# Kernel tuning notes

Hardware: AMD Instinct MI355X
Metric: run time of the kernel (lower is better)

## Reference

```python
import jax, jax.numpy as jnp
import numpy as np

VOCAB, X_SIZE, H_SIZE, N_CLASSES = 50000, 300, 150, 5
DEPTH = 18                      # complete binary tree, N = 2^(DEPTH+1)-1 nodes
N_NODES = 2 ** (DEPTH + 1) - 1  # 524287
SCALE = 0.05                    # param init scale for numerical sanity


def setup_inputs() -> dict:
    key = jax.random.key(0)
    ks = jax.random.split(key, 8)
    return {
        "x_id": jax.random.randint(ks[0], (N_NODES,), 0, VOCAB, dtype=jnp.int32),
        "emb": jax.random.normal(ks[1], (VOCAB, X_SIZE), jnp.float32) * SCALE,
        "W_iou": jax.random.normal(ks[2], (X_SIZE, 3 * H_SIZE), jnp.float32) * SCALE,
        "U_iou": jax.random.normal(ks[3], (H_SIZE, 3 * H_SIZE), jnp.float32) * SCALE,
        "b_iou": jnp.zeros((3 * H_SIZE,), jnp.float32),
        "W_f": jax.random.normal(ks[4], (X_SIZE, H_SIZE), jnp.float32) * SCALE,
        "U_f": jax.random.normal(ks[5], (H_SIZE, H_SIZE), jnp.float32) * SCALE,
        "b_f": jnp.zeros((H_SIZE,), jnp.float32),
        "W_out": jax.random.normal(ks[6], (H_SIZE, N_CLASSES), jnp.float32) * SCALE,
        "b_out": jnp.zeros((N_CLASSES,), jnp.float32),
    }


def reference(x_id, emb, W_iou, U_iou, b_iou, W_f, U_f, b_f, W_out, b_out):
    # Child-Sum TreeLSTM propagated leaves->root over a complete binary tree
    # stored in heap layout: children of node i are 2i+1, 2i+2.
    N = x_id.shape[0]
    H = U_iou.shape[0]
    depth = int(np.log2(N + 1)) - 1

    x = emb[x_id]  # input_module: embedding lookup  [N, X]
    h = jnp.zeros((N, H), x.dtype)
    c = jnp.zeros((N, H), x.dtype)

    # level-batched topological propagation (19 static levels)
    for lvl in range(depth, -1, -1):
        s, e = 2 ** lvl - 1, 2 ** (lvl + 1) - 1  # node range of this level
        xl = x[s:e]                              # [n_l, X]
        if lvl == depth:  # leaves: zero child state
            h_sum = jnp.zeros((e - s, H), x.dtype)
            fc_sum = jnp.zeros((e - s, H), x.dtype)
        else:
            # children of consecutive nodes are contiguous: [2s+1, 2e+1)
            hc = h[2 * s + 1:2 * e + 1].reshape(e - s, 2, H)
            cc = c[2 * s + 1:2 * e + 1].reshape(e - s, 2, H)
            h_sum = hc.sum(axis=1)               # reduce: sum child h
            # per-child forget gate
            f = jax.nn.sigmoid((xl @ W_f)[:, None, :] + hc @ U_f + b_f)
            fc_sum = (f * cc).sum(axis=1)
        iou = xl @ W_iou + h_sum @ U_iou + b_iou  # [n_l, 3H]
        i, o, u = jnp.split(iou, 3, axis=-1)
        c_new = jax.nn.sigmoid(i) * jnp.tanh(u) + fc_sum
        h_new = jax.nn.sigmoid(o) * jnp.tanh(c_new)
        h = h.at[s:e].set(h_new)
        c = c.at[s:e].set(c_new)

    return h @ W_out + b_out  # output_module: Linear(H, C)  [N, C]
```

## Files before the change

kernel.cpp:

```cpp
#include <hip/hip_runtime.h>
#include <cstdint>

typedef _Float16 f16_t;
typedef __attribute__((ext_vector_type(8))) _Float16 f16x8;
typedef __attribute__((ext_vector_type(4))) _Float16 f16x4;
typedef __attribute__((ext_vector_type(4))) float f32x4;

#define HP      160
#define NCOL    640
#define KXP     320
#define NNODES  524287
#define LEAF_S  262143
#define NVOCAB  50000
#define AST     168
#define BST     36
#define CST     162

__device__ __forceinline__ float frcp(float x) { return __builtin_amdgcn_rcpf(x); }
__device__ __forceinline__ float sigf(float x) { return frcp(1.0f + __expf(-x)); }
__device__ __forceinline__ float tanhf_(float x) {
  return 1.0f - 2.0f * frcp(1.0f + __expf(2.0f * x));
}
__device__ __forceinline__ f16x8 zero8() {
  f16x8 z;
#pragma unroll
  for (int i = 0; i < 8; ++i) z[i] = (_Float16)0.0f;
  return z;
}
__device__ __forceinline__ f32x4 zero4() {
  f32x4 z;
#pragma unroll
  for (int i = 0; i < 4; ++i) z[i] = 0.0f;
  return z;
}

__device__ __forceinline__ void stage_B(const f16_t* __restrict__ UreT, f16_t* B_sh,
                                        int tid, int j0, int kk) {
#pragma unroll
  for (int i = 0; i < 2; ++i) {
    int ch = tid + 256 * i;
    int cidx = ch >> 2, kc = (ch & 3) * 8;
    int g = cidx >> 5, jj = cidx & 31;
    int col = g * HP + j0 + jj;
    f16x8 v = *(const f16x8*)&UreT[col * HP + kk + kc];
    f16x4 lo = {v[0], v[1], v[2], v[3]};
    f16x4 hi = {v[4], v[5], v[6], v[7]};
    *(f16x4*)&B_sh[cidx * BST + kc] = lo;
    *(f16x4*)&B_sh[cidx * BST + kc + 4] = hi;
  }
}
__device__ __forceinline__ f16x8 read_B(const f16_t* B_sh, int tile16, int q) {
  f16x4 lo = *(const f16x4*)&B_sh[tile16 * BST + q * 8];
  f16x4 hi = *(const f16x4*)&B_sh[tile16 * BST + q * 8 + 4];
  f16x8 v = {lo[0], lo[1], lo[2], lo[3], hi[0], hi[1], hi[2], hi[3]};
  return v;
}

__global__ void prep_params(const float* __restrict__ W_iou, const float* __restrict__ U_iou,
                            const float* __restrict__ b_iou, const float* __restrict__ W_f,
                            const float* __restrict__ U_f, const float* __restrict__ b_f,
                            f16_t* __restrict__ WreT, f16_t* __restrict__ UreT,
                            float* __restrict__ bre) {
  int idx = blockIdx.x * 256 + threadIdx.x;
  if (idx < NCOL * KXP) {
    int col = idx / KXP, k = idx % KXP;
    int j = col >> 2, g = col & 3;
    float v = 0.0f;
    if (k < 300 && j < 150) v = (g < 3) ? W_iou[k * 450 + g * 150 + j] : W_f[k * 150 + j];
    WreT[idx] = (f16_t)v;
  } else if (idx < NCOL * KXP + NCOL * HP) {
    int i2 = idx - NCOL * KXP;
    int col = i2 / HP, k = i2 % HP;
    int g = col / 160, j = col % 160;
    float v = 0.0f;
    if (k < 150 && j < 150) v = (g < 3) ? U_iou[k * 450 + g * 150 + j] : U_f[k * 150 + j];
    UreT[i2] = (f16_t)v;
  } else if (idx < NCOL * KXP + NCOL * HP + NCOL) {
    int col = idx - (NCOL * KXP + NCOL * HP);
    int j = col >> 2, g = col & 3;
    bre[col] = (j < 150) ? ((g < 3) ? b_iou[g * 150 + j] : b_f[j]) : 0.0f;
  }
}

__global__ __launch_bounds__(256) void gemm_p(const float* __restrict__ emb,
                                              const f16_t* __restrict__ WreT,
                                              const float* __restrict__ bre,
                                              f16_t* __restrict__ P) {
  __shared__ __align__(16) f16_t A_sh[64 * 328];
  __shared__ __align__(16) f16_t B_sh[128 * 40];
  const int tid = threadIdx.x;
  const int wid = tid >> 6, lane = tid & 63, l15 = lane & 15, q = lane >> 4;
  const int row0 = blockIdx.x * 64;

#pragma unroll
  for (int i = 0; i < 10; ++i) {
    int ch = tid + 256 * i;
    int r = ch / 40, kc = (ch % 40) * 8;
    int grow = row0 + r;
    f16x8 hv;
    if (grow < NVOCAB && kc + 8 <= 300) {
      float4 a = *(const float4*)&emb[grow * 300 + kc];
      float4 b = *(const float4*)&emb[grow * 300 + kc + 4];
      hv[0] = (_Float16)a.x; hv[1] = (_Float16)a.y; hv[2] = (_Float16)a.z; hv[3] = (_Float16)a.w;
      hv[4] = (_Float16)b.x; hv[5] = (_Float16)b.y; hv[6] = (_Float16)b.z; hv[7] = (_Float16)b.w;
    } else {
#pragma unroll
      for (int e = 0; e < 8; ++e) {
        int k = kc + e;
        float v = (grow < NVOCAB && k < 300) ? emb[grow * 300 + k] : 0.0f;
        hv[e] = (_Float16)v;
      }
    }
    *(f16x8*)&A_sh[r * 328 + kc] = hv;
  }
  __syncthreads();

  for (int bn = 0; bn < 5; ++bn) {
    const int col0 = bn * 128;
    f32x4 acc[8];
#pragma unroll
    for (int t = 0; t < 8; ++t) acc[t] = zero4();
    for (int kk = 0; kk < KXP; kk += 32) {
#pragma unroll
      for (int i = 0; i < 2; ++i) {
        int ch = tid + 256 * i;
        int cidx = ch >> 2, kc = (ch & 3) * 8;
        *(f16x8*)&B_sh[cidx * 40 + kc] =
            *(const f16x8*)&WreT[(col0 + cidx) * KXP + kk + kc];
      }
      __syncthreads();
      f16x8 af = *(const f16x8*)&A_sh[(16 * wid + l15) * 328 + kk + q * 8];
#pragma unroll
      for (int t = 0; t < 8; ++t) {
        f16x8 bfr = *(const f16x8*)&B_sh[(t * 16 + l15) * 40 + q * 8];
        acc[t] = __builtin_amdgcn_mfma_f32_16x16x32_f16(af, bfr, acc[t], 0, 0, 0);
      }
      __syncthreads();
    }
#pragma unroll
    for (int t = 0; t < 8; ++t) {
      int col = col0 + t * 16 + l15;
      float bias = bre[col];
#pragma unroll
      for (int r2 = 0; r2 < 4; ++r2) {
        int row = row0 + 16 * wid + q * 4 + r2;
        if (row < NVOCAB) P[(long)row * NCOL + col] = (f16_t)(acc[t][r2] + bias);
      }
    }
  }
}

__global__ void leafhc_kernel(const f16_t* __restrict__ P, f16_t* __restrict__ Hleaf,
                              f16_t* __restrict__ Cleaf) {
  int idx = blockIdx.x * 256 + threadIdx.x;
  if (idx >= NVOCAB * 80) return;
  int v = idx / 80, t = idx % 80;
  f16x8 pk = *(const f16x8*)&P[(long)v * NCOL + t * 8];
#pragma unroll
  for (int e = 0; e < 2; ++e) {
    float iv = (float)pk[e * 4 + 0], ov = (float)pk[e * 4 + 1], uv = (float)pk[e * 4 + 2];
    float cl = sigf(iv) * tanhf_(uv);
    float hl = sigf(ov) * tanhf_(cl);
    Hleaf[(long)v * HP + t * 2 + e] = (f16_t)hl;
    Cleaf[(long)v * HP + t * 2 + e] = (f16_t)cl;
  }
}

__global__ __launch_bounds__(256, 3) void fused17_kernel(
    const int* __restrict__ x_id, const f16_t* __restrict__ P,
    const f16_t* __restrict__ UreT, const f16_t* __restrict__ Hleaf,
    const f16_t* __restrict__ Cleaf, f16_t* __restrict__ Hout,
    f16_t* __restrict__ Cout, const float* __restrict__ W_out,
    const float* __restrict__ b_out, float* __restrict__ out) {
  __shared__ __align__(16) f16_t A_sh[64 * AST];
  __shared__ __align__(16) f16_t A2_sh[32 * AST];
  __shared__ __align__(16) f16_t B_sh[128 * BST];
  __shared__ f16_t C_sh[32 * CST];
  __shared__ __align__(16) f16_t Wo16[160 * 8];
  const int tid = threadIdx.x;
  const int wid = tid >> 6, lane = tid & 63, l15 = lane & 15, q = lane >> 4;
  const int p0 = blockIdx.x * 32;
  const int s1 = (1 << 17) - 1;
  const long childbase = (long)LEAF_S + 2 * p0;

  for (int idx = tid; idx < 1280; idx += 256) {
    int j = idx >> 3, m = idx & 7;
    Wo16[idx] = (j < 150 && m < 5) ? (f16_t)W_out[j * 5 + m] : (f16_t)0.0f;
  }

#pragma unroll
  for (int i = 0; i < 5; ++i) {
    int ch = tid + 256 * i;
    int r = ch / 20, kc = (ch % 20) * 8;
    int xv = x_id[childbase + r];
    *(f16x8*)&A_sh[r * AST + kc] = *(const f16x8*)&Hleaf[(long)xv * HP + kc];
  }
  __syncthreads();

  {
    const int row = 16 * wid + l15;
    const int jb = q * 40;
    float o[5] = {0, 0, 0, 0, 0};
#pragma unroll
    for (int jc = 0; jc < 5; ++jc) {
      f16x8 hv8 = *(const f16x8*)&A_sh[row * AST + jb + jc * 8];
#pragma unroll
      for (int e = 0; e < 8; ++e) {
        float hv = (float)hv8[e];
        f16x8 w8 = *(const f16x8*)&Wo16[(jb + jc * 8 + e) * 8];
#pragma unroll
        for (int m = 0; m < 5; ++m) o[m] += hv * (float)w8[m];
      }
    }
#pragma unroll
    for (int m = 0; m < 5; ++m) {
      float v = o[m];
      v += __shfl_xor(v, 16);
      v += __shfl_xor(v, 32);
      o[m] = v;
    }
    if (q == 0) {
      long base = (childbase + row) * 5;
#pragma unroll
      for (int m = 0; m < 5; ++m) out[base + m] = o[m] + b_out[m];
    }
  }

  int xvp[2], xvl[2], xvr[2];
#pragma unroll
  for (int rr = 0; rr < 2; ++rr) {
    int pl = 8 * wid + 2 * q + rr;
    long pn = (long)s1 + p0 + pl;
    xvp[rr] = x_id[pn];
    xvl[rr] = x_id[childbase + 2 * pl];
    xvr[rr] = x_id[childbase + 2 * pl + 1];
  }

  for (int jt = 0; jt < 5; ++jt) {
    const int j0 = jt * 32;
    f32x4 acc[4][2];
#pragma unroll
    for (int g = 0; g < 4; ++g)
#pragma unroll
      for (int jh = 0; jh < 2; ++jh) acc[g][jh] = zero4();

    for (int kk = 0; kk < HP; kk += 32) {
      stage_B(UreT, B_sh, tid, j0, kk);
      __syncthreads();
      f16x8 af = *(const f16x8*)&A_sh[(16 * wid + l15) * AST + kk + q * 8];
#pragma unroll
      for (int g = 0; g < 4; ++g)
#pragma unroll
        for (int jh = 0; jh < 2; ++jh) {
          f16x8 bfr = read_B(B_sh, g * 32 + jh * 16 + l15, q);
          acc[g][jh] = __builtin_amdgcn_mfma_f32_16x16x32_f16(af, bfr, acc[g][jh], 0, 0, 0);
        }
      __syncthreads();
    }

#pragma unroll
    for (int rr = 0; rr < 2; ++rr) {
      const int r = rr * 2;
      const int pl = 8 * wid + 2 * q + rr;
      const f16_t* Prp = P + (long)xvp[rr] * NCOL;
      const f16_t* Prl = Cleaf + (long)xvl[rr] * HP;
      const f16_t* Prr_ = Cleaf + (long)xvr[rr] * HP;
#pragma unroll
      for (int jh = 0; jh < 2; ++jh) {
        const int j = j0 + jh * 16 + l15;
        f16x4 pp = *(const f16x4*)&Prp[j * 4];
        float ipre = (float)pp[0] + acc[0][jh][r] + acc[0][jh][r + 1];
        float opre = (float)pp[1] + acc[1][jh][r] + acc[1][jh][r + 1];
        float upre = (float)pp[2] + acc[2][jh][r] + acc[2][jh][r + 1];
        float pf   = (float)pp[3];
        float fl = sigf(pf + acc[3][jh][r]);
        float fr = sigf(pf + acc[3][jh][r + 1]);
        float clv = (float)Prl[j];
        float crv = (float)Prr_[j];
        float cn = sigf(ipre) * tanhf_(upre) + fl * clv + fr * crv;
        float hn = sigf(opre) * tanhf_(cn);
        A2_sh[pl * AST + j] = (f16_t)hn;
        C_sh[pl * CST + j] = (f16_t)cn;
      }
    }
  }
  __syncthreads();

  if (wid < 2) {
    const int row = 16 * wid + l15;
    const int jb = q * 40;
    float o[5] = {0, 0, 0, 0, 0};
#pragma unroll
    for (int jc = 0; jc < 5; ++jc) {
      f16x8 hv8 = *(const f16x8*)&A2_sh[row * AST + jb + jc * 8];
#pragma unroll
      for (int e = 0; e < 8; ++e) {
        float hv = (float)hv8[e];
        f16x8 w8 = *(const f16x8*)&Wo16[(jb + jc * 8 + e) * 8];
#pragma unroll
        for (int m = 0; m < 5; ++m) o[m] += hv * (float)w8[m];
      }
    }
#pragma unroll
    for (int m = 0; m < 5; ++m) {
      float v = o[m];
      v += __shfl_xor(v, 16);
      v += __shfl_xor(v, 32);
      o[m] = v;
    }
    if (q == 0) {
      long base = ((long)s1 + p0 + row) * 5;
#pragma unroll
      for (int m = 0; m < 5; ++m) out[base + m] = o[m] + b_out[m];
    }
  }

  const int s2 = (s1 - 1) >> 1;
  const int p02 = p0 >> 1;
  const bool act2 = (wid < 2);
  int xvp2[2];
#pragma unroll
  for (int rr = 0; rr < 2; ++rr) {
    int pl = 8 * wid + 2 * q + rr;
    long pn = (long)s2 + p02 + (act2 ? pl : 0);
    xvp2[rr] = x_id[pn];
  }

  for (int jt = 0; jt < 5; ++jt) {
    const int j0 = jt * 32;
    f32x4 acc[4][2];
#pragma unroll
    for (int g = 0; g < 4; ++g)
#pragma unroll
      for (int jh = 0; jh < 2; ++jh) acc[g][jh] = zero4();

    for (int kk = 0; kk < HP; kk += 32) {
      stage_B(UreT, B_sh, tid, j0, kk);
      __syncthreads();
      if (act2) {
        f16x8 af = *(const f16x8*)&A2_sh[(16 * wid + l15) * AST + kk + q * 8];
#pragma unroll
        for (int g = 0; g < 4; ++g)
#pragma unroll
          for (int jh = 0; jh < 2; ++jh) {
            f16x8 bfr = read_B(B_sh, g * 32 + jh * 16 + l15, q);
            acc[g][jh] = __builtin_amdgcn_mfma_f32_16x16x32_f16(af, bfr, acc[g][jh], 0, 0, 0);
          }
      }
      __syncthreads();
    }

    if (act2) {
#pragma unroll
      for (int rr = 0; rr < 2; ++rr) {
        const int r = rr * 2;
        const int lr0 = 16 * wid + q * 4 + r;
        const int pl = lr0 >> 1;
        const f16_t* Prp = P + (long)xvp2[rr] * NCOL;
#pragma unroll
        for (int jh = 0; jh < 2; ++jh) {
          const int j = j0 + jh * 16 + l15;
          f16x4 pp = *(const f16x4*)&Prp[j * 4];
          float ipre = (float)pp[0] + acc[0][jh][r] + acc[0][jh][r + 1];
          float opre = (float)pp[1] + acc[1][jh][r] + acc[1][jh][r + 1];
          float upre = (float)pp[2] + acc[2][jh][r] + acc[2][jh][r + 1];
          float pf   = (float)pp[3];
          float fl = sigf(pf + acc[3][jh][r]);
          float fr = sigf(pf + acc[3][jh][r + 1]);
          float clv = (float)C_sh[lr0 * CST + j];
          float crv = (float)C_sh[(lr0 + 1) * CST + j];
          float cn = sigf(ipre) * tanhf_(upre) + fl * clv + fr * crv;
          float hn = sigf(opre) * tanhf_(cn);
          Hout[(long)(p02 + pl) * HP + j] = (f16_t)hn;
          Cout[(long)(p02 + pl) * HP + j] = (f16_t)cn;
        }
      }
    }
  }
}

__global__ __launch_bounds__(256, 4) void level_k(
    const int* __restrict__ x_id, const f16_t* __restrict__ P,
    const f16_t* __restrict__ UreT, const f16_t* __restrict__ Hc,
    const f16_t* __restrict__ Cc, f16_t* __restrict__ Hp,
    f16_t* __restrict__ Cp, const float* __restrict__ W_out,
    const float* __restrict__ b_out, float* __restrict__ out, int s, int M) {
  __shared__ __align__(16) f16_t A_sh[64 * AST];
  __shared__ __align__(16) f16_t B_sh[128 * BST];
  __shared__ __align__(16) float Wo[160 * 8];
  const int tid = threadIdx.x;
  const int wid = tid >> 6, lane = tid & 63, l15 = lane & 15, q = lane >> 4;
  const int p0 = blockIdx.x * 32;
  const long childbase = 2L * s + 1 + 2 * p0;

  for (int idx = tid; idx < 1280; idx += 256) {
    int j = idx >> 3, m = idx & 7;
    Wo[idx] = (j < 150 && m < 5) ? W_out[j * 5 + m] : 0.0f;
  }

#pragma unroll
  for (int i = 0; i < 5; ++i) {
    int ch = tid + 256 * i;
    int r = ch / 20, kc = (ch % 20) * 8;
    *(f16x8*)&A_sh[r * AST + kc] = *(const f16x8*)&Hc[(long)(2 * p0 + r) * HP + kc];
  }
  __syncthreads();

  {
    const int row = 16 * wid + l15;
    const int jb = q * 40;
    float o[5] = {0, 0, 0, 0, 0};
#pragma unroll
    for (int jc = 0; jc < 5; ++jc) {
      f16x8 hv8 = *(const f16x8*)&A_sh[row * AST + jb + jc * 8];
#pragma unroll
      for (int e = 0; e < 8; ++e) {
        float hv = (float)hv8[e];
        int j = jb + jc * 8 + e;
        float4 w4 = *(const float4*)&Wo[j * 8];
        float w5 = Wo[j * 8 + 4];
        o[0] += hv * w4.x; o[1] += hv * w4.y; o[2] += hv * w4.z;
        o[3] += hv * w4.w; o[4] += hv * w5;
      }
    }
#pragma unroll
    for (int m = 0; m < 5; ++m) {
      float v = o[m];
      v += __shfl_xor(v, 16);
      v += __shfl_xor(v, 32);
      o[m] = v;
    }
    if (q == 0) {
      long base = (childbase + row) * 5;
#pragma unroll
      for (int m = 0; m < 5; ++m) out[base + m] = o[m] + b_out[m];
    }
  }

  int xvp[2];
#pragma unroll
  for (int rr = 0; rr < 2; ++rr) {
    int pl = 8 * wid + 2 * q + rr;
    xvp[rr] = x_id[(long)s + p0 + pl];
  }

  for (int jt = 0; jt < 5; ++jt) {
    const int j0 = jt * 32;
    f32x4 acc[4][2];
#pragma unroll
    for (int g = 0; g < 4; ++g)
#pragma unroll
      for (int jh = 0; jh < 2; ++jh) acc[g][jh] = zero4();

    for (int kk = 0; kk < HP; kk += 32) {
      stage_B(UreT, B_sh, tid, j0, kk);
      __syncthreads();
      f16x8 af = *(const f16x8*)&A_sh[(16 * wid + l15) * AST + kk + q * 8];
#pragma unroll
      for (int g = 0; g < 4; ++g)
#pragma unroll
        for (int jh = 0; jh < 2; ++jh) {
          f16x8 bfr = read_B(B_sh, g * 32 + jh * 16 + l15, q);
          acc[g][jh] = __builtin_amdgcn_mfma_f32_16x16x32_f16(af, bfr, acc[g][jh], 0, 0, 0);
        }
      __syncthreads();
    }

#pragma unroll
    for (int rr = 0; rr < 2; ++rr) {
      const int r = rr * 2;
      const int lr0 = 16 * wid + q * 4 + r;
      const int pl = lr0 >> 1;
      const f16_t* Prp = P + (long)xvp[rr] * NCOL;
#pragma unroll
      for (int jh = 0; jh < 2; ++jh) {
        const int j = j0 + jh * 16 + l15;
        f16x4 pp = *(const f16x4*)&Prp[j * 4];
        float ipre = (float)pp[0] + acc[0][jh][r] + acc[0][jh][r + 1];
        float opre = (float)pp[1] + acc[1][jh][r] + acc[1][jh][r + 1];
        float upre = (float)pp[2] + acc[2][jh][r] + acc[2][jh][r + 1];
        float pf   = (float)pp[3];
        float fl = sigf(pf + acc[3][jh][r]);
        float fr = sigf(pf + acc[3][jh][r + 1]);
        float clv = (float)Cc[(long)(2 * p0 + lr0) * HP + j];
        float crv = (float)Cc[(long)(2 * p0 + lr0 + 1) * HP + j];
        float cn = sigf(ipre) * tanhf_(upre) + fl * clv + fr * crv;
        float hn = sigf(opre) * tanhf_(cn);
        Hp[(long)(p0 + pl) * HP + j] = (f16_t)hn;
        Cp[(long)(p0 + pl) * HP + j] = (f16_t)cn;
      }
    }
  }
}

__global__ __launch_bounds__(256, 4) void tail_kernel(
    const int* __restrict__ x_id, const f16_t* __restrict__ P,
    const f16_t* __restrict__ UreT, f16_t* __restrict__ HX, f16_t* __restrict__ HY,
    f16_t* __restrict__ CX, f16_t* __restrict__ CY, const float* __restrict__ W_out,
    const float* __restrict__ b_out, float* __restrict__ out) {
  __shared__ __align__(16) f16_t A_sh[64 * AST];
  __shared__ __align__(16) f16_t B_sh[128 * BST];
  __shared__ __align__(16) float Wo[160 * 8];
  const int tid = threadIdx.x;
  const int wid = tid >> 6, lane = tid & 63, l15 = lane & 15, q = lane >> 4;

  for (int idx = tid; idx < 1280; idx += 256) {
    int j = idx >> 3, m = idx & 7;
    Wo[idx] = (j < 150 && m < 5) ? W_out[j * 5 + m] : 0.0f;
  }

  for (int lvl = 5; lvl >= 0; --lvl) {
    const int s = (1 << lvl) - 1, M = 1 << lvl;
    const f16_t* hc = (lvl & 1) ? HX : HY;
    const f16_t* cc = (lvl & 1) ? CX : CY;
    f16_t* hp = (lvl & 1) ? HY : HX;
    f16_t* cp = (lvl & 1) ? CY : CX;
    int rowsValid = 2 * M;
    if (rowsValid > 64) rowsValid = 64;

    __syncthreads();
#pragma unroll
    for (int i = 0; i < 5; ++i) {
      int ch = tid + 256 * i;
      int r = ch / 20, kc = (ch % 20) * 8;
      f16x8 v = (r < rowsValid) ? *(const f16x8*)&hc[(long)r * HP + kc] : zero8();
      *(f16x8*)&A_sh[r * AST + kc] = v;
    }
    __syncthreads();

    {
      const int row = 16 * wid + l15;
      if (row < rowsValid) {
        const int jb = q * 40;
        float o[5] = {0, 0, 0, 0, 0};
#pragma unroll
        for (int jc = 0; jc < 5; ++jc) {
          f16x8 hv8 = *(const f16x8*)&A_sh[row * AST + jb + jc * 8];
#pragma unroll
          for (int e = 0; e < 8; ++e) {
            float hv = (float)hv8[e];
            int j = jb + jc * 8 + e;
            float4 w4 = *(const float4*)&Wo[j * 8];
            float w5 = Wo[j * 8 + 4];
            o[0] += hv * w4.x; o[1] += hv * w4.y; o[2] += hv * w4.z;
            o[3] += hv * w4.w; o[4] += hv * w5;
          }
        }
#pragma unroll
        for (int m = 0; m < 5; ++m) {
          float v = o[m];
          v += __shfl_xor(v, 16);
          v += __shfl_xor(v, 32);
          o[m] = v;
        }
        if (q == 0) {
          long base = (long)(2 * s + 1 + row) * 5;
#pragma unroll
          for (int m = 0; m < 5; ++m) out[base + m] = o[m] + b_out[m];
        }
      }
    }

    int xvp[2]; bool valid[2];
#pragma unroll
    for (int rr = 0; rr < 2; ++rr) {
      int pl = 8 * wid + 2 * q + rr;
      valid[rr] = pl < M;
      xvp[rr] = x_id[(long)s + (valid[rr] ? pl : 0)];
    }

    for (int jt = 0; jt < 5; ++jt) {
      const int j0 = jt * 32;
      f32x4 acc[4][2];
#pragma unroll
      for (int g = 0; g < 4; ++g)
#pragma unroll
        for (int jh = 0; jh < 2; ++jh) acc[g][jh] = zero4();

      for (int kk = 0; kk < HP; kk += 32) {
        stage_B(UreT, B_sh, tid, j0, kk);
        __syncthreads();
        f16x8 af = *(const f16x8*)&A_sh[(16 * wid + l15) * AST + kk + q * 8];
#pragma unroll
        for (int g = 0; g < 4; ++g)
#pragma unroll
          for (int jh = 0; jh < 2; ++jh) {
            f16x8 bfr = read_B(B_sh, g * 32 + jh * 16 + l15, q);
            acc[g][jh] = __builtin_amdgcn_mfma_f32_16x16x32_f16(af, bfr, acc[g][jh], 0, 0, 0);
          }
        __syncthreads();
      }

#pragma unroll
      for (int rr = 0; rr < 2; ++rr) {
        const int r = rr * 2;
        const int lr0 = 16 * wid + q * 4 + r;
        const int pl = lr0 >> 1;
        const f16_t* Prp = P + (long)xvp[rr] * NCOL;
#pragma unroll
        for (int jh = 0; jh < 2; ++jh) {
          const int j = j0 + jh * 16 + l15;
          f16x4 pp = *(const f16x4*)&Prp[j * 4];
          float ipre = (float)pp[0] + acc[0][jh][r] + acc[0][jh][r + 1];
          float opre = (float)pp[1] + acc[1][jh][r] + acc[1][jh][r + 1];
          float upre = (float)pp[2] + acc[2][jh][r] + acc[2][jh][r + 1];
          float pf   = (float)pp[3];
          float fl = sigf(pf + acc[3][jh][r]);
          float fr = sigf(pf + acc[3][jh][r + 1]);
          float clv = valid[rr] ? (float)cc[(long)lr0 * HP + j] : 0.0f;
          float crv = valid[rr] ? (float)cc[(long)(lr0 + 1) * HP + j] : 0.0f;
          float cn = sigf(ipre) * tanhf_(upre) + fl * clv + fr * crv;
          float hn = sigf(opre) * tanhf_(cn);
          if (valid[rr]) {
            hp[(long)pl * HP + j] = (f16_t)hn;
            cp[(long)pl * HP + j] = (f16_t)cn;
          }
        }
      }
    }
    __threadfence();
  }

  __threadfence();
  __syncthreads();
  if (tid < 64) {
    float o[5] = {0, 0, 0, 0, 0};
    for (int j = tid; j < 150; j += 64) {
      float hv = (float)HX[j];
      float4 w4 = *(const float4*)&Wo[j * 8];
      float w5 = Wo[j * 8 + 4];
      o[0] += hv * w4.x; o[1] += hv * w4.y; o[2] += hv * w4.z;
      o[3] += hv * w4.w; o[4] += hv * w5;
    }
#pragma unroll
    for (int m = 0; m < 5; ++m) {
      float v = o[m];
      v += __shfl_xor(v, 1);
      v += __shfl_xor(v, 2);
      v += __shfl_xor(v, 4);
      v += __shfl_xor(v, 8);
      v += __shfl_xor(v, 16);
      v += __shfl_xor(v, 32);
      o[m] = v;
    }
    if (tid == 0) {
#pragma unroll
      for (int m = 0; m < 5; ++m) out[m] = o[m] + b_out[m];
    }
  }
}

extern "C" void kernel_launch(void* const* d_in, const int* in_sizes, int n_in,
                              void* d_out, int out_size, void* d_ws, size_t ws_size,
                              hipStream_t stream) {
  const int* x_id   = (const int*)d_in[0];
  const float* emb  = (const float*)d_in[1];
  const float* W_iou = (const float*)d_in[2];
  const float* U_iou = (const float*)d_in[3];
  const float* b_iou = (const float*)d_in[4];
  const float* W_f   = (const float*)d_in[5];
  const float* U_f   = (const float*)d_in[6];
  const float* b_f   = (const float*)d_in[7];
  const float* W_out = (const float*)d_in[8];
  const float* b_out = (const float*)d_in[9];
  float* out = (float*)d_out;
  char* ws = (char*)d_ws;

  f16_t* WreT  = (f16_t*)(ws + 0);
  f16_t* UreT  = (f16_t*)(ws + 409600);
  float* bre   = (float*)(ws + 614400);
  f16_t* P     = (f16_t*)(ws + 616960);
  f16_t* Hleaf = (f16_t*)(ws + 64616960);
  f16_t* Cleaf = (f16_t*)(ws + 80616960);
  f16_t* HX    = (f16_t*)(ws + 96616960);
  f16_t* HY    = (f16_t*)(ws + 117588480);
  f16_t* CX    = (f16_t*)(ws + 138560000);
  f16_t* CY    = (f16_t*)(ws + 159531520);

  prep_params<<<1203, 256, 0, stream>>>(W_iou, U_iou, b_iou, W_f, U_f, b_f, WreT, UreT, bre);
  gemm_p<<<782, 256, 0, stream>>>(emb, WreT, bre, P);
  leafhc_kernel<<<15625, 256, 0, stream>>>(P, Hleaf, Cleaf);

  fused17_kernel<<<4096, 256, 0, stream>>>(x_id, P, UreT, Hleaf, Cleaf, HX, CX,
                                           W_out, b_out, out);

  for (int L = 15; L >= 6; --L) {
    int s = (1 << L) - 1, M = 1 << L;
    const f16_t* hc = (L & 1) ? HX : HY;
    const f16_t* cc = (L & 1) ? CX : CY;
    f16_t* hp = (L & 1) ? HY : HX;
    f16_t* cp = (L & 1) ? CY : CX;
    level_k<<<M / 32, 256, 0, stream>>>(x_id, P, UreT, hc, cc, hp, cp,
                                        W_out, b_out, out, s, M);
  }

  tail_kernel<<<1, 256, 0, stream>>>(x_id, P, UreT, HX, HY, CX, CY, W_out, b_out, out);

  (void)in_sizes; (void)n_in; (void)out_size; (void)ws_size;
}
```

Before: 896.5 us.

## Keep child h in registers and fuse output projection into gate epilogues

Child h rows for the MFMA A operand are now loaded straight from global memory into registers, so the A_sh shared tile and its staging pass go away. The output Linear for each node is computed inside the gate epilogue, using the freshly produced h and a shuffle reduction, instead of a separate pass over the children at the next level. Dropping the shared tile lets the launch bound for the fused kernel rise from 3 to 4 blocks per SM. The trade-off is more register pressure, and the output head's weights move to fp16 in the per-level kernels.

```diff
diff --git a/kernel.cpp b/kernel.cpp
--- a/kernel.cpp
+++ b/kernel.cpp
@@ -9,7 +9,6 @@
 #define HP      160
 #define NCOL    640
 #define KXP     320
-#define NNODES  524287
 #define LEAF_S  262143
 #define NVOCAB  50000
 #define AST     168
@@ -166,15 +165,14 @@
   }
 }
 
-__global__ __launch_bounds__(256, 3) void fused17_kernel(
+__global__ __launch_bounds__(256, 4) void fused17_kernel(
     const int* __restrict__ x_id, const f16_t* __restrict__ P,
     const f16_t* __restrict__ UreT, const f16_t* __restrict__ Hleaf,
     const f16_t* __restrict__ Cleaf, f16_t* __restrict__ Hout,
     f16_t* __restrict__ Cout, const float* __restrict__ W_out,
     const float* __restrict__ b_out, float* __restrict__ out) {
-  __shared__ __align__(16) f16_t A_sh[64 * AST];
+  __shared__ __align__(16) f16_t B_sh[128 * BST];
   __shared__ __align__(16) f16_t A2_sh[32 * AST];
-  __shared__ __align__(16) f16_t B_sh[128 * BST];
   __shared__ f16_t C_sh[32 * CST];
   __shared__ __align__(16) f16_t Wo16[160 * 8];
   const int tid = threadIdx.x;
@@ -188,30 +186,35 @@
     Wo16[idx] = (j < 150 && m < 5) ? (f16_t)W_out[j * 5 + m] : (f16_t)0.0f;
   }
 
-#pragma unroll
-  for (int i = 0; i < 5; ++i) {
-    int ch = tid + 256 * i;
-    int r = ch / 20, kc = (ch % 20) * 8;
-    int xv = x_id[childbase + r];
-    *(f16x8*)&A_sh[r * AST + kc] = *(const f16x8*)&Hleaf[(long)xv * HP + kc];
+  const int row = 16 * wid + l15;
+  const int xvrow = x_id[childbase + row];
+  const f16_t* hrow = Hleaf + (long)xvrow * HP;
+  f16x8 areg[5];
+#pragma unroll
+  for (int kx = 0; kx < 5; ++kx) areg[kx] = *(const f16x8*)&hrow[kx * 32 + q * 8];
+
+  int xvp[2], xvl[2], xvr[2];
+#pragma unroll
+  for (int rr = 0; rr < 2; ++rr) {
+    int pl = 8 * wid + 2 * q + rr;
+    xvp[rr] = x_id[(long)s1 + p0 + pl];
+    xvl[rr] = x_id[childbase + 2 * pl];
+    xvr[rr] = x_id[childbase + 2 * pl + 1];
   }
   __syncthreads();
 
   {
-    const int row = 16 * wid + l15;
-    const int jb = q * 40;
     float o[5] = {0, 0, 0, 0, 0};
 #pragma unroll
-    for (int jc = 0; jc < 5; ++jc) {
-      f16x8 hv8 = *(const f16x8*)&A_sh[row * AST + jb + jc * 8];
+    for (int kx = 0; kx < 5; ++kx)
 #pragma unroll
       for (int e = 0; e < 8; ++e) {
-        float hv = (float)hv8[e];
-        f16x8 w8 = *(const f16x8*)&Wo16[(jb + jc * 8 + e) * 8];
+        int j = kx * 32 + q * 8 + e;
+        float hv = (float)areg[kx][e];
+        f16x8 w8 = *(const f16x8*)&Wo16[j * 8];
 #pragma unroll
         for (int m = 0; m < 5; ++m) o[m] += hv * (float)w8[m];
       }
-    }
 #pragma unroll
     for (int m = 0; m < 5; ++m) {
       float v = o[m];
@@ -226,16 +229,7 @@
     }
   }
 
-  int xvp[2], xvl[2], xvr[2];
-#pragma unroll
-  for (int rr = 0; rr < 2; ++rr) {
-    int pl = 8 * wid + 2 * q + rr;
-    long pn = (long)s1 + p0 + pl;
-    xvp[rr] = x_id[pn];
-    xvl[rr] = x_id[childbase + 2 * pl];
-    xvr[rr] = x_id[childbase + 2 * pl + 1];
-  }
-
+  float oacc1[2][5] = {};
   for (int jt = 0; jt < 5; ++jt) {
     const int j0 = jt * 32;
     f32x4 acc[4][2];
@@ -244,16 +238,15 @@
 #pragma unroll
       for (int jh = 0; jh < 2; ++jh) acc[g][jh] = zero4();
 
-    for (int kk = 0; kk < HP; kk += 32) {
-      stage_B(UreT, B_sh, tid, j0, kk);
-      __syncthreads();
-      f16x8 af = *(const f16x8*)&A_sh[(16 * wid + l15) * AST + kk + q * 8];
+    for (int kx = 0; kx < 5; ++kx) {
+      stage_B(UreT, B_sh, tid, j0, kx * 32);
+      __syncthreads();
 #pragma unroll
       for (int g = 0; g < 4; ++g)
 #pragma unroll
         for (int jh = 0; jh < 2; ++jh) {
           f16x8 bfr = read_B(B_sh, g * 32 + jh * 16 + l15, q);
-          acc[g][jh] = __builtin_amdgcn_mfma_f32_16x16x32_f16(af, bfr, acc[g][jh], 0, 0, 0);
+          acc[g][jh] = __builtin_amdgcn_mfma_f32_16x16x32_f16(areg[kx], bfr, acc[g][jh], 0, 0, 0);
         }
       __syncthreads();
     }
@@ -263,8 +256,8 @@
       const int r = rr * 2;
       const int pl = 8 * wid + 2 * q + rr;
       const f16_t* Prp = P + (long)xvp[rr] * NCOL;
-      const f16_t* Prl = Cleaf + (long)xvl[rr] * HP;
-      const f16_t* Prr_ = Cleaf + (long)xvr[rr] * HP;
+      const f16_t* Crl = Cleaf + (long)xvl[rr] * HP;
+      const f16_t* Crr = Cleaf + (long)xvr[rr] * HP;
 #pragma unroll
       for (int jh = 0; jh < 2; ++jh) {
         const int j = j0 + jh * 16 + l15;
@@ -275,57 +268,49 @@
         float pf   = (float)pp[3];
         float fl = sigf(pf + acc[3][jh][r]);
         float fr = sigf(pf + acc[3][jh][r + 1]);
-        float clv = (float)Prl[j];
-        float crv = (float)Prr_[j];
-        float cn = sigf(ipre) * tanhf_(upre) + fl * clv + fr * crv;
+        float cn = sigf(ipre) * tanhf_(upre) + fl * (float)Crl[j] + fr * (float)Crr[j];
         float hn = sigf(opre) * tanhf_(cn);
         A2_sh[pl * AST + j] = (f16_t)hn;
         C_sh[pl * CST + j] = (f16_t)cn;
+        f16x8 w8 = *(const f16x8*)&Wo16[j * 8];
+#pragma unroll
+        for (int m = 0; m < 5; ++m) oacc1[rr][m] += hn * (float)w8[m];
       }
     }
   }
   __syncthreads();
 
-  if (wid < 2) {
-    const int row = 16 * wid + l15;
-    const int jb = q * 40;
-    float o[5] = {0, 0, 0, 0, 0};
-#pragma unroll
-    for (int jc = 0; jc < 5; ++jc) {
-      f16x8 hv8 = *(const f16x8*)&A2_sh[row * AST + jb + jc * 8];
-#pragma unroll
-      for (int e = 0; e < 8; ++e) {
-        float hv = (float)hv8[e];
-        f16x8 w8 = *(const f16x8*)&Wo16[(jb + jc * 8 + e) * 8];
-#pragma unroll
-        for (int m = 0; m < 5; ++m) o[m] += hv * (float)w8[m];
-      }
-    }
+#pragma unroll
+  for (int rr = 0; rr < 2; ++rr) {
+    const int pl = 8 * wid + 2 * q + rr;
 #pragma unroll
     for (int m = 0; m < 5; ++m) {
-      float v = o[m];
-      v += __shfl_xor(v, 16);
-      v += __shfl_xor(v, 32);
-      o[m] = v;
-    }
-    if (q == 0) {
-      long base = ((long)s1 + p0 + row) * 5;
-#pragma unroll
-      for (int m = 0; m < 5; ++m) out[base + m] = o[m] + b_out[m];
+      float v = oacc1[rr][m];
+      v += __shfl_xor(v, 1);
+      v += __shfl_xor(v, 2);
+      v += __shfl_xor(v, 4);
+      v += __shfl_xor(v, 8);
+      if (l15 == 0) out[((long)s1 + p0 + pl) * 5 + m] = v + b_out[m];
     }
   }
 
   const int s2 = (s1 - 1) >> 1;
   const int p02 = p0 >> 1;
   const bool act2 = (wid < 2);
+  f16x8 a2reg[5];
+  if (act2) {
+#pragma unroll
+    for (int kx = 0; kx < 5; ++kx)
+      a2reg[kx] = *(const f16x8*)&A2_sh[(16 * wid + l15) * AST + kx * 32 + q * 8];
+  }
   int xvp2[2];
 #pragma unroll
   for (int rr = 0; rr < 2; ++rr) {
     int pl = 8 * wid + 2 * q + rr;
-    long pn = (long)s2 + p02 + (act2 ? pl : 0);
-    xvp2[rr] = x_id[pn];
-  }
-
+    xvp2[rr] = x_id[(long)s2 + p02 + (act2 ? pl : 0)];
+  }
+
+  float oacc2[2][5] = {};
   for (int jt = 0; jt < 5; ++jt) {
     const int j0 = jt * 32;
     f32x4 acc[4][2];
@@ -334,17 +319,16 @@
 #pragma unroll
       for (int jh = 0; jh < 2; ++jh) acc[g][jh] = zero4();
 
-    for (int kk = 0; kk < HP; kk += 32) {
-      stage_B(UreT, B_sh, tid, j0, kk);
+    for (int kx = 0; kx < 5; ++kx) {
+      stage_B(UreT, B_sh, tid, j0, kx * 32);
       __syncthreads();
       if (act2) {
-        f16x8 af = *(const f16x8*)&A2_sh[(16 * wid + l15) * AST + kk + q * 8];
 #pragma unroll
         for (int g = 0; g < 4; ++g)
 #pragma unroll
           for (int jh = 0; jh < 2; ++jh) {
             f16x8 bfr = read_B(B_sh, g * 32 + jh * 16 + l15, q);
-            acc[g][jh] = __builtin_amdgcn_mfma_f32_16x16x32_f16(af, bfr, acc[g][jh], 0, 0, 0);
+            acc[g][jh] = __builtin_amdgcn_mfma_f32_16x16x32_f16(a2reg[kx], bfr, acc[g][jh], 0, 0, 0);
           }
       }
       __syncthreads();
@@ -367,13 +351,31 @@
           float pf   = (float)pp[3];
           float fl = sigf(pf + acc[3][jh][r]);
           float fr = sigf(pf + acc[3][jh][r + 1]);
-          float clv = (float)C_sh[lr0 * CST + j];
-          float crv = (float)C_sh[(lr0 + 1) * CST + j];
-          float cn = sigf(ipre) * tanhf_(upre) + fl * clv + fr * crv;
+          float cn = sigf(ipre) * tanhf_(upre) +
+                     fl * (float)C_sh[lr0 * CST + j] + fr * (float)C_sh[(lr0 + 1) * CST + j];
           float hn = sigf(opre) * tanhf_(cn);
           Hout[(long)(p02 + pl) * HP + j] = (f16_t)hn;
           Cout[(long)(p02 + pl) * HP + j] = (f16_t)cn;
+          f16x8 w8 = *(const f16x8*)&Wo16[j * 8];
+#pragma unroll
+          for (int m = 0; m < 5; ++m) oacc2[rr][m] += hn * (float)w8[m];
         }
+      }
+    }
+  }
+
+  if (act2) {
+#pragma unroll
+    for (int rr = 0; rr < 2; ++rr) {
+      const int pl = 8 * wid + 2 * q + rr;
+#pragma unroll
+      for (int m = 0; m < 5; ++m) {
+        float v = oacc2[rr][m];
+        v += __shfl_xor(v, 1);
+        v += __shfl_xor(v, 2);
+        v += __shfl_xor(v, 4);
+        v += __shfl_xor(v, 8);
+        if (l15 == 0) out[((long)s2 + p02 + pl) * 5 + m] = v + b_out[m];
       }
     }
   }
@@ -385,57 +387,22 @@
     const f16_t* __restrict__ Cc, f16_t* __restrict__ Hp,
     f16_t* __restrict__ Cp, const float* __restrict__ W_out,
     const float* __restrict__ b_out, float* __restrict__ out, int s, int M) {
-  __shared__ __align__(16) f16_t A_sh[64 * AST];
   __shared__ __align__(16) f16_t B_sh[128 * BST];
-  __shared__ __align__(16) float Wo[160 * 8];
+  __shared__ __align__(16) f16_t Wo16[160 * 8];
   const int tid = threadIdx.x;
   const int wid = tid >> 6, lane = tid & 63, l15 = lane & 15, q = lane >> 4;
   const int p0 = blockIdx.x * 32;
-  const long childbase = 2L * s + 1 + 2 * p0;
 
   for (int idx = tid; idx < 1280; idx += 256) {
     int j = idx >> 3, m = idx & 7;
-    Wo[idx] = (j < 150 && m < 5) ? W_out[j * 5 + m] : 0.0f;
-  }
-
-#pragma unroll
-  for (int i = 0; i < 5; ++i) {
-    int ch = tid + 256 * i;
-    int r = ch / 20, kc = (ch % 20) * 8;
-    *(f16x8*)&A_sh[r * AST + kc] = *(const f16x8*)&Hc[(long)(2 * p0 + r) * HP + kc];
-  }
-  __syncthreads();
-
-  {
-    const int row = 16 * wid + l15;
-    const int jb = q * 40;
-    float o[5] = {0, 0, 0, 0, 0};
-#pragma unroll
-    for (int jc = 0; jc < 5; ++jc) {
-      f16x8 hv8 = *(const f16x8*)&A_sh[row * AST + jb + jc * 8];
-#pragma unroll
-      for (int e = 0; e < 8; ++e) {
-        float hv = (float)hv8[e];
-        int j = jb + jc * 8 + e;
-        float4 w4 = *(const float4*)&Wo[j * 8];
-        float w5 = Wo[j * 8 + 4];
-        o[0] += hv * w4.x; o[1] += hv * w4.y; o[2] += hv * w4.z;
-        o[3] += hv * w4.w; o[4] += hv * w5;
-      }
-    }
-#pragma unroll
-    for (int m = 0; m < 5; ++m) {
-      float v = o[m];
-      v += __shfl_xor(v, 16);
-      v += __shfl_xor(v, 32);
-      o[m] = v;
-    }
-    if (q == 0) {
-      long base = (childbase + row) * 5;
-#pragma unroll
-      for (int m = 0; m < 5; ++m) out[base + m] = o[m] + b_out[m];
-    }
-  }
+    Wo16[idx] = (j < 150 && m < 5) ? (f16_t)W_out[j * 5 + m] : (f16_t)0.0f;
+  }
+
+  const int row = 16 * wid + l15;
+  const f16_t* hrow = Hc + (long)(2 * p0 + row) * HP;
+  f16x8 areg[5];
+#pragma unroll
+  for (int kx = 0; kx < 5; ++kx) areg[kx] = *(const f16x8*)&hrow[kx * 32 + q * 8];
 
   int xvp[2];
 #pragma unroll
@@ -443,7 +410,9 @@
     int pl = 8 * wid + 2 * q + rr;
     xvp[rr] = x_id[(long)s + p0 + pl];
   }
-
+  __syncthreads();
+
+  float oacc[2][5] = {};
   for (int jt = 0; jt < 5; ++jt) {
     const int j0 = jt * 32;
     f32x4 acc[4][2];
@@ -452,16 +421,15 @@
 #pragma unroll
       for (int jh = 0; jh < 2; ++jh) acc[g][jh] = zero4();
 
-    for (int kk = 0; kk < HP; kk += 32) {
-      stage_B(UreT, B_sh, tid, j0, kk);
-      __syncthreads();
-      f16x8 af = *(const f16x8*)&A_sh[(16 * wid + l15) * AST + kk + q * 8];
+    for (int kx = 0; kx < 5; ++kx) {
+      stage_B(UreT, B_sh, tid, j0, kx * 32);
+      __syncthreads();
 #pragma unroll
       for (int g = 0; g < 4; ++g)
 #pragma unroll
         for (int jh = 0; jh < 2; ++jh) {
           f16x8 bfr = read_B(B_sh, g * 32 + jh * 16 + l15, q);
-          acc[g][jh] = __builtin_amdgcn_mfma_f32_16x16x32_f16(af, bfr, acc[g][jh], 0, 0, 0);
+          acc[g][jh] = __builtin_amdgcn_mfma_f32_16x16x32_f16(areg[kx], bfr, acc[g][jh], 0, 0, 0);
         }
       __syncthreads();
     }
@@ -488,7 +456,24 @@
         float hn = sigf(opre) * tanhf_(cn);
         Hp[(long)(p0 + pl) * HP + j] = (f16_t)hn;
         Cp[(long)(p0 + pl) * HP + j] = (f16_t)cn;
-      }
+        f16x8 w8 = *(const f16x8*)&Wo16[j * 8];
+#pragma unroll
+        for (int m = 0; m < 5; ++m) oacc[rr][m] += hn * (float)w8[m];
+      }
+    }
+  }
+
+#pragma unroll
+  for (int rr = 0; rr < 2; ++rr) {
+    const int pl = 8 * wid + 2 * q + rr;
+#pragma unroll
+    for (int m = 0; m < 5; ++m) {
+      float v = oacc[rr][m];
+      v += __shfl_xor(v, 1);
+      v += __shfl_xor(v, 2);
+      v += __shfl_xor(v, 4);
+      v += __shfl_xor(v, 8);
+      if (l15 == 0) out[((long)s + p0 + pl) * 5 + m] = v + b_out[m];
     }
   }
 }
@@ -498,15 +483,14 @@
     const f16_t* __restrict__ UreT, f16_t* __restrict__ HX, f16_t* __restrict__ HY,
     f16_t* __restrict__ CX, f16_t* __restrict__ CY, const float* __restrict__ W_out,
     const float* __restrict__ b_out, float* __restrict__ out) {
-  __shared__ __align__(16) f16_t A_sh[64 * AST];
   __shared__ __align__(16) f16_t B_sh[128 * BST];
-  __shared__ __align__(16) float Wo[160 * 8];
+  __shared__ __align__(16) f16_t Wo16[160 * 8];
   const int tid = threadIdx.x;
   const int wid = tid >> 6, lane = tid & 63, l15 = lane & 15, q = lane >> 4;
 
   for (int idx = tid; idx < 1280; idx += 256) {
     int j = idx >> 3, m = idx & 7;
-    Wo[idx] = (j < 150 && m < 5) ? W_out[j * 5 + m] : 0.0f;
+    Wo16[idx] = (j < 150 && m < 5) ? (f16_t)W_out[j * 5 + m] : (f16_t)0.0f;
   }
 
   for (int lvl = 5; lvl >= 0; --lvl) {
@@ -518,48 +502,15 @@
     int rowsValid = 2 * M;
     if (rowsValid > 64) rowsValid = 64;
 
+    __threadfence();
     __syncthreads();
-#pragma unroll
-    for (int i = 0; i < 5; ++i) {
-      int ch = tid + 256 * i;
-      int r = ch / 20, kc = (ch % 20) * 8;
-      f16x8 v = (r < rowsValid) ? *(const f16x8*)&hc[(long)r * HP + kc] : zero8();
-      *(f16x8*)&A_sh[r * AST + kc] = v;
-    }
-    __syncthreads();
-
-    {
-      const int row = 16 * wid + l15;
-      if (row < rowsValid) {
-        const int jb = q * 40;
-        float o[5] = {0, 0, 0, 0, 0};
-#pragma unroll
-        for (int jc = 0; jc < 5; ++jc) {
-          f16x8 hv8 = *(const f16x8*)&A_sh[row * AST + jb + jc * 8];
-#pragma unroll
-          for (int e = 0; e < 8; ++e) {
-            float hv = (float)hv8[e];
-            int j = jb + jc * 8 + e;
-            float4 w4 = *(const float4*)&Wo[j * 8];
-            float w5 = Wo[j * 8 + 4];
-            o[0] += hv * w4.x; o[1] += hv * w4.y; o[2] += hv * w4.z;
-            o[3] += hv * w4.w; o[4] += hv * w5;
-          }
-        }
-#pragma unroll
-        for (int m = 0; m < 5; ++m) {
-          float v = o[m];
-          v += __shfl_xor(v, 16);
-          v += __shfl_xor(v, 32);
-          o[m] = v;
-        }
-        if (q == 0) {
-          long base = (long)(2 * s + 1 + row) * 5;
-#pragma unroll
-          for (int m = 0; m < 5; ++m) out[base + m] = o[m] + b_out[m];
-        }
-      }
-    }
+
+    const int row = 16 * wid + l15;
+    f16x8 areg[5];
+#pragma unroll
+    for (int kx = 0; kx < 5; ++kx)
+      areg[kx] = (row < rowsValid) ? *(const f16x8*)&hc[(long)row * HP + kx * 32 + q * 8]
+                                   : zero8();
 
     int xvp[2]; bool valid[2];
 #pragma unroll
@@ -569,6 +520,7 @@
       xvp[rr] = x_id[(long)s + (valid[rr] ? pl : 0)];
     }
 
+    float oacc[2][5] = {};
     for (int jt = 0; jt < 5; ++jt) {
       const int j0 = jt * 32;
       f32x4 acc[4][2];
@@ -577,16 +529,15 @@
 #pragma unroll
         for (int jh = 0; jh < 2; ++jh) acc[g][jh] = zero4();
 
-      for (int kk = 0; kk < HP; kk += 32) {
-        stage_B(UreT, B_sh, tid, j0, kk);
+      for (int kx = 0; kx < 5; ++kx) {
+        stage_B(UreT, B_sh, tid, j0, kx * 32);
         __syncthreads();
-        f16x8 af = *(const f16x8*)&A_sh[(16 * wid + l15) * AST + kk + q * 8];
 #pragma unroll
         for (int g = 0; g < 4; ++g)
 #pragma unroll
           for (int jh = 0; jh < 2; ++jh) {
             f16x8 bfr = read_B(B_sh, g * 32 + jh * 16 + l15, q);
-            acc[g][jh] = __builtin_amdgcn_mfma_f32_16x16x32_f16(af, bfr, acc[g][jh], 0, 0, 0);
+            acc[g][jh] = __builtin_amdgcn_mfma_f32_16x16x32_f16(areg[kx], bfr, acc[g][jh], 0, 0, 0);
           }
         __syncthreads();
       }
@@ -615,37 +566,25 @@
             hp[(long)pl * HP + j] = (f16_t)hn;
             cp[(long)pl * HP + j] = (f16_t)cn;
           }
+          f16x8 w8 = *(const f16x8*)&Wo16[j * 8];
+#pragma unroll
+          for (int m = 0; m < 5; ++m) oacc[rr][m] += hn * (float)w8[m];
         }
       }
     }
-    __threadfence();
-  }
-
-  __threadfence();
-  __syncthreads();
-  if (tid < 64) {
-    float o[5] = {0, 0, 0, 0, 0};
-    for (int j = tid; j < 150; j += 64) {
-      float hv = (float)HX[j];
-      float4 w4 = *(const float4*)&Wo[j * 8];
-      float w5 = Wo[j * 8 + 4];
-      o[0] += hv * w4.x; o[1] += hv * w4.y; o[2] += hv * w4.z;
-      o[3] += hv * w4.w; o[4] += hv * w5;
-    }
-#pragma unroll
-    for (int m = 0; m < 5; ++m) {
-      float v = o[m];
-      v += __shfl_xor(v, 1);
-      v += __shfl_xor(v, 2);
-      v += __shfl_xor(v, 4);
-      v += __shfl_xor(v, 8);
-      v += __shfl_xor(v, 16);
-      v += __shfl_xor(v, 32);
-      o[m] = v;
-    }
-    if (tid == 0) {
-#pragma unroll
-      for (int m = 0; m < 5; ++m) out[m] = o[m] + b_out[m];
+
+#pragma unroll
+    for (int rr = 0; rr < 2; ++rr) {
+      const int pl = 8 * wid + 2 * q + rr;
+#pragma unroll
+      for (int m = 0; m < 5; ++m) {
+        float v = oacc[rr][m];
+        v += __shfl_xor(v, 1);
+        v += __shfl_xor(v, 2);
+        v += __shfl_xor(v, 4);
+        v += __shfl_xor(v, 8);
+        if (l15 == 0 && valid[rr]) out[((long)s + pl) * 5 + m] = v + b_out[m];
+      }
     }
   }
 }
```

After: 885.1 us. About the same (-1.3%).
